# Kernel tuning notes

Measured on AMD Instinct MI355X. Metric: run time of the kernel, lower is better.

Reference implementation:

```python
import jax, jax.numpy as jnp
import numpy as np

BETA = 0.9
ITER = 2


def setup_inputs() -> dict:
    key = jax.random.key(0)
    B, items, E = 8, 32, 128
    N = B * items * items  # 8192 pairs
    k1, k2 = jax.random.split(key)
    pairs = jax.random.normal(k1, (N, E), dtype=jnp.float32)
    # scale W so bilinear scores don't saturate sigmoid (init faithfulness not required)
    W = jax.random.normal(k2, (E, E), dtype=jnp.float32) / jnp.sqrt(jnp.float32(E))
    cond = jnp.ones((B, items, items), dtype=jnp.int32)  # all pairs valid (dense nonzero)
    # map_pair[b,i,j] = row-major linear index into `pairs`, matching torch.nonzero order
    map_pair = jnp.arange(N, dtype=jnp.int32).reshape(B, items, items)
    return {"pairs": pairs, "W": W, "cond": cond, "map_pair": map_pair}


def reference(pairs, W, cond, map_pair):
    B, items = map_pair.shape[0], map_pair.shape[1]
    N, E = pairs.shape
    # torch.nonzero of the broadcast [B,items,items,items] cond; cond is dense (all nonzero),
    # so nonzeros enumerate all (b,i,j,k) in row-major order.
    bi, ii, ji, ki = [x.reshape(-1) for x in jnp.indices((B, items, items, items))]
    part1 = map_pair[bi, ii, ki]  # pair (i,k)
    part2 = map_pair[bi, ki, ji]  # pair (k,j)
    valid = (part1 >= 0) & (part2 >= 0)  # [N*items]
    # static -inf masks (loop-invariant)
    eq_mask = ((ji == ki) | (ii == ki)).reshape(N, items)  # idx2==idx3 or idx1==idx3
    ar = jnp.arange(items)
    diag_idx = map_pair[:, ar, ar].reshape(-1)  # self-pairs (i,i) -> rows of N
    row_mask = jnp.zeros((N,), dtype=bool).at[diag_idx].set(True)
    inf_mask = eq_mask | row_mask[:, None]  # [N, items]
    neg_inf = jnp.float32(-jnp.inf)

    for _ in range(ITER):
        # generate: bilinear then gather
        bilin = pairs @ W  # [N, E]
        a = jnp.where(valid[:, None], bilin[part1], 0.0).reshape(N, items, E)
        b = jnp.where(valid[:, None], pairs[part2], 0.0).reshape(N, items, E)
        new_pairs = a * b  # [N, items, E]
        # aggregate: masked -inf fills
        new_pairs = jnp.where(inf_mask[:, :, None], neg_inf, new_pairs)
        zero_mask = jnp.all(new_pairs == 0.0, axis=2)  # [N, items]
        new_pairs = jnp.where(zero_mask[:, :, None], neg_inf, new_pairs)
        # interpolation gate: 1 where all walks are masked, beta otherwise
        mat = jnp.where(jnp.all(jnp.isinf(new_pairs), axis=1), 1.0, jnp.float32(BETA))  # [N, E]
        new = jnp.sum(jax.nn.sigmoid(new_pairs), axis=1)  # sigmoid(-inf)=0; [N, E]
        pairs = mat * pairs + (1.0 - mat) * new
    return pairs
```

## Files before the change

### kernel.cpp

```cpp
#include <hip/hip_runtime.h>

typedef __attribute__((ext_vector_type(8))) short bf16x8;
typedef __attribute__((ext_vector_type(4))) float f32x4;

#define NEG_LOG2E (-1.4426950408889634f)

__device__ __forceinline__ short f2bf(float f) {
    unsigned u = __float_as_uint(f);
    unsigned r = (u + 0x7FFFu + ((u >> 16) & 1u)) >> 16;
    return (short)r;
}

__global__ __launch_bounds__(256) void prep(
    const float* __restrict__ pairs,
    const float* __restrict__ W,
    short* __restrict__ pbf,
    short* __restrict__ WTs)
{
    const int t = threadIdx.x, blk = blockIdx.x;
    if (blk < 64) {
        int idx = blk * 256 + t;
        int k = idx >> 7, n = idx & 127;
        WTs[n * 128 + k] = f2bf(NEG_LOG2E * W[idx]);
    } else {
        int f = (blk - 64) * 256 + t;
        float4 v = ((const float4*)pairs)[f];
        union { short s[4]; unsigned long long u; } pk;
        pk.s[0] = f2bf(v.x); pk.s[1] = f2bf(v.y);
        pk.s[2] = f2bf(v.z); pk.s[3] = f2bf(v.w);
        *(unsigned long long*)(pbf + (size_t)f * 4) = pk.u;
    }
}

__global__ __launch_bounds__(512, 4) void walk_iter(
    const float* __restrict__ srcF,
    const short* __restrict__ srcB,
    const short* __restrict__ WTs,
    float* __restrict__ dstF,
    short* __restrict__ dstB)
{
    __shared__ float G[32][132];

    const int t  = threadIdx.x;
    const int blk = blockIdx.x;
    const int b  = blk & 7;
    const int i  = (blk >> 3) & 31;
    const int jg = blk >> 8;
    const int bi = b * 32 + i;

    const int j  = jg * 16 + (t >> 5);
    const int g  = t & 31, e0 = g << 2;

    const float* pb = srcF + ((size_t)(b * 1024) + j) * 128 + e0;
    float4 ring[4];
    ring[0] = *(const float4*)(pb);
    ring[1] = *(const float4*)(pb + 4096);
    ring[2] = *(const float4*)(pb + 2 * 4096);
    ring[3] = *(const float4*)(pb + 3 * 4096);

    {
        const int wv = t >> 6, l = t & 63;
        const int m0 = (wv & 1) * 16;
        const int lm = l & 15, quad = l >> 4;
        const int n0 = (wv >> 1) * 16;
        const short* arow = srcB + (size_t)(bi * 32 + m0 + lm) * 128;
        const short* brow = WTs + (size_t)(n0 + lm) * 128;
        f32x4 acc0 = {0.f, 0.f, 0.f, 0.f};
        f32x4 acc1 = {0.f, 0.f, 0.f, 0.f};
        #pragma unroll
        for (int kb = 0; kb < 4; ++kb) {
            int ko = kb * 32 + quad * 8;
            bf16x8 af  = *(const bf16x8*)(arow + ko);
            bf16x8 bf0 = *(const bf16x8*)(brow + ko);
            bf16x8 bf1 = *(const bf16x8*)(brow + 64 * 128 + ko);
            acc0 = __builtin_amdgcn_mfma_f32_16x16x32_bf16(af, bf0, acc0, 0, 0, 0);
            acc1 = __builtin_amdgcn_mfma_f32_16x16x32_bf16(af, bf1, acc1, 0, 0, 0);
        }
        #pragma unroll
        for (int r = 0; r < 4; ++r) {
            G[m0 + quad * 4 + r][n0 + lm]      = acc0[r];
            G[m0 + quad * 4 + r][n0 + 64 + lm] = acc1[r];
        }
    }
    __syncthreads();

    float4 sacc = make_float4(0.f, 0.f, 0.f, 0.f);
    if (i != j) {
        float4 gg = *(const float4*)&G[0][e0];
        #pragma unroll
        for (int k = 0; k < 32; ++k) {
            float4 p = ring[k & 3];
            if (k + 4 < 32)
                ring[k & 3] = *(const float4*)(pb + (size_t)(k + 4) * 4096);
            float4 gn;
            if (k + 1 < 32) gn = *(const float4*)&G[k + 1][e0];
            float t0 = gg.x * p.x, t1 = gg.y * p.y;
            float t2 = gg.z * p.z, t3 = gg.w * p.w;
            float x0 = __builtin_amdgcn_exp2f(t0);
            float x1 = __builtin_amdgcn_exp2f(t1);
            float x2 = __builtin_amdgcn_exp2f(t2);
            float x3 = __builtin_amdgcn_exp2f(t3);
            float d0 = 1.0f + x0, d1 = 1.0f + x1;
            float d2 = 1.0f + x2, d3 = 1.0f + x3;
            float d01 = d0 * d1, d23 = d2 * d3;
            float r = __builtin_amdgcn_rcpf(d01 * d23);
            r = ((k == i) | (k == j)) ? 0.0f : r;
            float r01 = r * d23, r23 = r * d01;
            sacc.x = fmaf(r01, d1, sacc.x);
            sacc.y = fmaf(r01, d0, sacc.y);
            sacc.z = fmaf(r23, d3, sacc.z);
            sacc.w = fmaf(r23, d2, sacc.w);
            gg = gn;
        }
    }

    const float matv = (i == j) ? 1.0f : 0.9f;
    const float om   = 1.0f - matv;
    const size_t orow = ((size_t)bi * 32 + j) * 128 + e0;
    float4 pr = *(const float4*)(srcF + orow);
    float4 o;
    o.x = fmaf(om, sacc.x, matv * pr.x);
    o.y = fmaf(om, sacc.y, matv * pr.y);
    o.z = fmaf(om, sacc.z, matv * pr.z);
    o.w = fmaf(om, sacc.w, matv * pr.w);
    *(float4*)(dstF + orow) = o;

    if (dstB) {
        union { short s[4]; unsigned long long u; } pk;
        pk.s[0] = f2bf(o.x); pk.s[1] = f2bf(o.y);
        pk.s[2] = f2bf(o.z); pk.s[3] = f2bf(o.w);
        *(unsigned long long*)(dstB + orow) = pk.u;
    }
}

extern "C" void kernel_launch(void* const* d_in, const int* in_sizes, int n_in,
                              void* d_out, int out_size, void* d_ws, size_t ws_size,
                              hipStream_t stream) {
    (void)in_sizes; (void)n_in; (void)out_size; (void)ws_size;
    const float* pairs = (const float*)d_in[0];
    const float* W     = (const float*)d_in[1];
    char* ws = (char*)d_ws;
    short* WTs   = (short*)ws;
    short* pbf   = (short*)(ws + (1 << 16));
    float* tmp   = (float*)(ws + (1 << 16) + (1 << 21));
    short* tmpbf = (short*)(ws + (1 << 16) + (1 << 21) + (1 << 22));
    float* out = (float*)d_out;

    prep<<<1088, 256, 0, stream>>>(pairs, W, pbf, WTs);
    walk_iter<<<512, 512, 0, stream>>>(pairs, pbf, WTs, tmp, tmpbf);
    walk_iter<<<512, 512, 0, stream>>>(tmp,   tmpbf, WTs, out, nullptr);
}
```

Measured before the change: 98.64 us.

## Fuse bf16 conversion of pairs and W into walk kernel, drop prep launch

Removes the separate prep kernel. Each walk_iter block now converts W into a transposed, pre-scaled bf16 tile in shared memory, and converts its fp32 pairs rows to bf16 on the fly for the MFMA. This also removes the bf16 side-output write in the first iteration. It saves one launch and the intermediate bf16 buffers, at the cost of every block redundantly loading and transposing the 64KB W and holding an extra ~34KB of LDS, which may reduce occupancy.

```diff
diff --git a/kernel.cpp b/kernel.cpp
--- a/kernel.cpp
+++ b/kernel.cpp
@@ -11,42 +11,20 @@
     return (short)r;
 }
 
-__global__ __launch_bounds__(256) void prep(
-    const float* __restrict__ pairs,
-    const float* __restrict__ W,
-    short* __restrict__ pbf,
-    short* __restrict__ WTs)
-{
-    const int t = threadIdx.x, blk = blockIdx.x;
-    if (blk < 64) {
-        int idx = blk * 256 + t;
-        int k = idx >> 7, n = idx & 127;
-        WTs[n * 128 + k] = f2bf(NEG_LOG2E * W[idx]);
-    } else {
-        int f = (blk - 64) * 256 + t;
-        float4 v = ((const float4*)pairs)[f];
-        union { short s[4]; unsigned long long u; } pk;
-        pk.s[0] = f2bf(v.x); pk.s[1] = f2bf(v.y);
-        pk.s[2] = f2bf(v.z); pk.s[3] = f2bf(v.w);
-        *(unsigned long long*)(pbf + (size_t)f * 4) = pk.u;
-    }
-}
-
 __global__ __launch_bounds__(512, 4) void walk_iter(
     const float* __restrict__ srcF,
-    const short* __restrict__ srcB,
-    const short* __restrict__ WTs,
-    float* __restrict__ dstF,
-    short* __restrict__ dstB)
+    const float* __restrict__ W,
+    float* __restrict__ dstF)
 {
+    __shared__ short Wt[128][136];
     __shared__ float G[32][132];
 
-    const int t  = threadIdx.x;
+    const int t   = threadIdx.x;
     const int blk = blockIdx.x;
-    const int b  = blk & 7;
-    const int i  = (blk >> 3) & 31;
-    const int jg = blk >> 8;
-    const int bi = b * 32 + i;
+    const int b   = blk & 7;
+    const int i   = (blk >> 3) & 31;
+    const int jg  = blk >> 8;
+    const int bi  = b * 32 + i;
 
     const int j  = jg * 16 + (t >> 5);
     const int g  = t & 31, e0 = g << 2;
@@ -58,21 +36,39 @@
     ring[2] = *(const float4*)(pb + 2 * 4096);
     ring[3] = *(const float4*)(pb + 3 * 4096);
 
+    #pragma unroll
+    for (int q = 0; q < 8; ++q) {
+        int f = t + 512 * q;
+        int k = f >> 5, n0 = (f & 31) << 2;
+        float4 v = *(const float4*)(W + (size_t)f * 4);
+        Wt[n0 + 0][k] = f2bf(NEG_LOG2E * v.x);
+        Wt[n0 + 1][k] = f2bf(NEG_LOG2E * v.y);
+        Wt[n0 + 2][k] = f2bf(NEG_LOG2E * v.z);
+        Wt[n0 + 3][k] = f2bf(NEG_LOG2E * v.w);
+    }
+    __syncthreads();
+
     {
         const int wv = t >> 6, l = t & 63;
         const int m0 = (wv & 1) * 16;
         const int lm = l & 15, quad = l >> 4;
         const int n0 = (wv >> 1) * 16;
-        const short* arow = srcB + (size_t)(bi * 32 + m0 + lm) * 128;
-        const short* brow = WTs + (size_t)(n0 + lm) * 128;
+        const float* arow = srcF + (size_t)(bi * 32 + m0 + lm) * 128;
         f32x4 acc0 = {0.f, 0.f, 0.f, 0.f};
         f32x4 acc1 = {0.f, 0.f, 0.f, 0.f};
         #pragma unroll
         for (int kb = 0; kb < 4; ++kb) {
             int ko = kb * 32 + quad * 8;
-            bf16x8 af  = *(const bf16x8*)(arow + ko);
-            bf16x8 bf0 = *(const bf16x8*)(brow + ko);
-            bf16x8 bf1 = *(const bf16x8*)(brow + 64 * 128 + ko);
+            float4 a0 = *(const float4*)(arow + ko);
+            float4 a1 = *(const float4*)(arow + ko + 4);
+            union { short s[8]; bf16x8 v; } pk;
+            pk.s[0] = f2bf(a0.x); pk.s[1] = f2bf(a0.y);
+            pk.s[2] = f2bf(a0.z); pk.s[3] = f2bf(a0.w);
+            pk.s[4] = f2bf(a1.x); pk.s[5] = f2bf(a1.y);
+            pk.s[6] = f2bf(a1.z); pk.s[7] = f2bf(a1.w);
+            bf16x8 af  = pk.v;
+            bf16x8 bf0 = *(const bf16x8*)&Wt[n0 + lm][ko];
+            bf16x8 bf1 = *(const bf16x8*)&Wt[n0 + 64 + lm][ko];
             acc0 = __builtin_amdgcn_mfma_f32_16x16x32_bf16(af, bf0, acc0, 0, 0, 0);
             acc1 = __builtin_amdgcn_mfma_f32_16x16x32_bf16(af, bf1, acc1, 0, 0, 0);
         }
@@ -124,13 +120,6 @@
     o.z = fmaf(om, sacc.z, matv * pr.z);
     o.w = fmaf(om, sacc.w, matv * pr.w);
     *(float4*)(dstF + orow) = o;
-
-    if (dstB) {
-        union { short s[4]; unsigned long long u; } pk;
-        pk.s[0] = f2bf(o.x); pk.s[1] = f2bf(o.y);
-        pk.s[2] = f2bf(o.z); pk.s[3] = f2bf(o.w);
-        *(unsigned long long*)(dstB + orow) = pk.u;
-    }
 }
 
 extern "C" void kernel_launch(void* const* d_in, const int* in_sizes, int n_in,
@@ -139,14 +128,9 @@
     (void)in_sizes; (void)n_in; (void)out_size; (void)ws_size;
     const float* pairs = (const float*)d_in[0];
     const float* W     = (const float*)d_in[1];
-    char* ws = (char*)d_ws;
-    short* WTs   = (short*)ws;
-    short* pbf   = (short*)(ws + (1 << 16));
-    float* tmp   = (float*)(ws + (1 << 16) + (1 << 21));
-    short* tmpbf = (short*)(ws + (1 << 16) + (1 << 21) + (1 << 22));
+    float* tmp = (float*)d_ws;
     float* out = (float*)d_out;
 
-    prep<<<1088, 256, 0, stream>>>(pairs, W, pbf, WTs);
-    walk_iter<<<512, 512, 0, stream>>>(pairs, pbf, WTs, tmp, tmpbf);
-    walk_iter<<<512, 512, 0, stream>>>(tmp,   tmpbf, WTs, out, nullptr);
+    walk_iter<<<512, 512, 0, stream>>>(pairs, W, tmp);
+    walk_iter<<<512, 512, 0, stream>>>(tmp,   W, out);
 }
```

Result: faster. 92.99 us (-5.7%).
